# Optimization experiments

Hardware: AMD Instinct MI355X
Metric: run time of the kernel (lower is better)

## Reference

```python
import jax, jax.numpy as jnp
import numpy as np
from jax import lax

TAU = 1.0
GUMBEL_SCALE = 1e-4
SEARCH_SPACE = [1, 2, 4, 8, 16, 32, 64]


def synth_weight(weight, alphas_after):
    """Per-block circulant projection of weight for each block size, mixed by alphas.

    weight: [O, I, k, k]. For block size b: reshape to (q,b,p,b,k,k), rotate rows so
    each circulant diagonal aligns, mean over the block row axis, broadcast back with
    the reverse rotation, and accumulate alpha-weighted.
    """
    O, I, k, _ = weight.shape
    w = alphas_after[0] * weight  # block_size == 1 -> identity
    for idx, b in enumerate(SEARCH_SPACE[1:], start=1):
        q, p = O // b, I // b
        tmp = weight.reshape(q, b, p, b, k, k).transpose(0, 2, 1, 3, 4, 5)  # q,p,b,b,k,k
        ii = jnp.arange(b)[:, None]
        jj = jnp.arange(b)[None, :]
        rot = tmp[:, :, ii, (ii + jj) % b]          # q,p,b,b,k,k : rotate_mat gather
        cir = rot.mean(axis=2)                       # q,p,b,k,k   : circulant mean
        out = cir[:, :, (jj - ii) % b]               # q,p,b,b,k,k : rev_rotate_mat gather
        out = out.transpose(0, 2, 1, 3, 4, 5).reshape(O, I, k, k)
        w = w + alphas_after[idx] * out
    return w


def setup_inputs() -> dict:
    key = jax.random.key(0)
    k1, k2, k3 = jax.random.split(key, 3)
    B, C, H = 16, 256, 56
    O, I, K = 256, 256, 3
    x = jax.random.normal(k1, (B, C, H, H), dtype=jnp.float32)
    # kaiming-uniform-ish init: uniform in [-bound, bound], bound = sqrt(6/fan_in)
    fan_in = I * K * K
    bound = float(np.sqrt(6.0 / fan_in))
    weight = jax.random.uniform(k2, (O, I, K, K), dtype=jnp.float32, minval=-bound, maxval=bound)
    alphas = jnp.ones((len(SEARCH_SPACE),), dtype=jnp.float32)
    gumbels = jax.random.normal(k3, (len(SEARCH_SPACE),), dtype=jnp.float32)
    return {"x": x, "weight": weight, "alphas": alphas, "gumbels": gumbels}


def reference(x, weight, alphas, gumbels):
    # gumbel_softmax with tiny Gumbel(0, 1e-4) noise (noise passed in for determinism)
    alphas_after = jax.nn.softmax((alphas + GUMBEL_SCALE * gumbels) / TAU, axis=-1)
    w = synth_weight(weight, alphas_after)
    k = weight.shape[-1]
    pad = k // 2
    stride = 1
    out = lax.conv_general_dilated(
        x, w,
        window_strides=(stride, stride),
        padding=[(pad, pad), (pad, pad)],
        dimension_numbers=("NCHW", "OIHW", "NCHW"),
    )
    return out
```

## Files before the change

### kernel.cpp

```cpp
#include <hip/hip_runtime.h>
#include <hip/hip_bf16.h>

typedef __attribute__((ext_vector_type(8))) short bf16x8;
typedef __attribute__((ext_vector_type(4))) float f32x4;

#define WR_OFF   27557888

#define BAND     24576
#define WBUF_OFF 49152
#define WBUF_SZ  16384

__global__ void diagsum_kernel(const float* __restrict__ W, float* __restrict__ S) {
    int t = blockIdx.x * 256 + threadIdx.x;
    int idx, n, lvlOff;
    if (t < 32768)      { idx = 1; n = t;          lvlOff = 0; }
    else if (t < 49152) { idx = 2; n = t - 32768;  lvlOff = 294912; }
    else if (t < 57344) { idx = 3; n = t - 49152;  lvlOff = 442368; }
    else if (t < 61440) { idx = 4; n = t - 57344;  lvlOff = 516096; }
    else if (t < 63488) { idx = 5; n = t - 61440;  lvlOff = 552960; }
    else                { idx = 6; n = t - 63488;  lvlOff = 571392; }
    int b = 1 << idx;
    int d = n & (b - 1);
    int qp = n >> idx;
    int p = qp & ((256 >> idx) - 1);
    int q = qp >> (8 - idx);
    float s[9];
    #pragma unroll
    for (int tp = 0; tp < 9; ++tp) s[tp] = 0.f;
    for (int tt = 0; tt < b; ++tt) {
        const float* wp = W + ((size_t)((q * b + tt) * 256 + p * b + ((tt + d) & (b - 1)))) * 9;
        #pragma unroll
        for (int tp = 0; tp < 9; ++tp) s[tp] += wp[tp];
    }
    float* o = S + (size_t)lvlOff + (size_t)n * 9;
    #pragma unroll
    for (int tp = 0; tp < 9; ++tp) o[tp] = s[tp];
}

__global__ void wsynth_kernel(const float* __restrict__ W,
                              const float* __restrict__ alphas,
                              const float* __restrict__ gumbels,
                              const float* __restrict__ S,
                              __hip_bfloat16* __restrict__ Wr) {
    int tid = blockIdx.x * 256 + threadIdx.x;
    int o = tid >> 8, i = tid & 255;

    float a[7]; float mx = -1e30f;
    for (int j = 0; j < 7; ++j) { a[j] = alphas[j] + 1.0e-4f * gumbels[j]; mx = fmaxf(mx, a[j]); }
    float s = 0.f;
    for (int j = 0; j < 7; ++j) { a[j] = __expf(a[j] - mx); s += a[j]; }
    float invs = 1.0f / s;
    for (int j = 0; j < 7; ++j) a[j] *= invs;

    float acc[9];
    const float* w0 = W + ((size_t)(o * 256 + i)) * 9;
    #pragma unroll
    for (int t = 0; t < 9; ++t) acc[t] = a[0] * w0[t];

    const int lvlOff[7] = {0, 0, 294912, 442368, 516096, 552960, 571392};
    int dif = i - o;
    #pragma unroll
    for (int idx = 1; idx < 7; ++idx) {
        int b = 1 << idx;
        int q = o >> idx, p = i >> idx, d = dif & (b - 1);
        int n = ((q * (256 >> idx) + p) << idx) + d;
        const float* sp = S + lvlOff[idx] + (size_t)n * 9;
        float sc = a[idx] / (float)b;
        #pragma unroll
        for (int tp = 0; tp < 9; ++tp) acc[tp] += sc * sp[tp];
    }
    #pragma unroll
    for (int tp = 0; tp < 9; ++tp)
        Wr[((size_t)(tp * 256 + o)) * 256 + i] = __float2bfloat16(acc[tp]);
}

__global__ void zero_border_kernel(__hip_bfloat16* __restrict__ Xp) {
    int t = blockIdx.x * 256 + threadIdx.x;
    int c = t & 255;
    int pp = t >> 8;
    int b = pp / 228;
    int p = pp - b * 228;
    int y, x;
    if (p < 58)       { y = 0;            x = p; }
    else if (p < 116) { y = 57;           x = p - 58; }
    else if (p < 172) { y = 1 + (p - 116); x = 0; }
    else              { y = 1 + (p - 172); x = 57; }
    Xp[((size_t)(b * 58 + y) * 58 + x) * 256 + c] = __float2bfloat16(0.f);
}

__global__ void pad_nhwc_kernel(const float* __restrict__ x,
                                __hip_bfloat16* __restrict__ Xp) {
    __shared__ float t[64][65];
    int p0 = blockIdx.x * 64;
    int c0 = blockIdx.y * 64;
    int b  = blockIdx.z;
    int lane = threadIdx.x & 63;
    int grp  = threadIdx.x >> 6;

    const float* src = x + ((size_t)(b * 256 + c0)) * 3136 + p0;
    #pragma unroll
    for (int it = 0; it < 16; ++it) {
        int c = it * 4 + grp;
        t[c][lane] = src[(size_t)c * 3136 + lane];
    }
    __syncthreads();
    #pragma unroll
    for (int it = 0; it < 16; ++it) {
        int pl = it * 4 + grp;
        int P = p0 + pl;
        int y = P / 56, xx = P - y * 56;
        Xp[(((size_t)(b * 58 + y + 1)) * 58 + (xx + 1)) * 256 + c0 + lane] =
            __float2bfloat16(t[lane][pl]);
    }
}

__device__ __forceinline__ void gload16(const __hip_bfloat16* g, char* l) {
    __builtin_amdgcn_global_load_lds(
        (const __attribute__((address_space(1))) void*)g,
        (__attribute__((address_space(3))) void*)l, 16, 0, 0);
}

template<int N> __device__ __forceinline__ void gate() {
    if constexpr (N == 0)      asm volatile("s_waitcnt vmcnt(0)" ::: "memory");
    else if constexpr (N == 2) asm volatile("s_waitcnt vmcnt(2)" ::: "memory");
    else if constexpr (N == 4) asm volatile("s_waitcnt vmcnt(4)" ::: "memory");
    else if constexpr (N == 7) asm volatile("s_waitcnt vmcnt(7)" ::: "memory");
}

template<bool LAST>
__device__ __forceinline__ void chunk_body(
    int cc, char* smem,
    const int (&aOff)[4], const int (&bOff)[7],
    const __hip_bfloat16* wSrc0, const __hip_bfloat16* const (&xSrc)[3],
    int tid, f32x4 (&acc)[4][7])
{
    const char* xb = smem + (cc & 1) * BAND;
    #pragma unroll
    for (int r = 0; r < 9; ++r) {
        if (!LAST || r <= 5) {
            const int tap2 = (r < 6) ? r + 3 : r - 6;
            const int cc2  = (r < 6) ? cc : cc + 1;
            const __hip_bfloat16* s = wSrc0 + tap2 * 65536 + cc2 * 32;
            char* d = smem + WBUF_OFF + ((cc + r + 3) & 3) * WBUF_SZ + tid * 16;
            gload16(s, d);
            gload16(s + 16, d + 8192);
        }
        if (!LAST && r == 3) {
            char* d = smem + ((cc + 1) & 1) * BAND + tid * 16;
            #pragma unroll
            for (int it = 0; it < 3; ++it)
                gload16(xSrc[it] + (cc + 1) * 32, d + it * 8192);
        }
        const char* wb = smem + WBUF_OFF + ((cc + r) & 3) * WBUF_SZ;
        const int dy = r / 3 - 1, dx = r % 3 - 1;
        const int timm = (dy * 64 + dx) * 16;
        bf16x8 af[4], bfv[7];
        #pragma unroll
        for (int nf = 0; nf < 4; ++nf) af[nf] = *(const bf16x8*)(wb + aOff[nf]);
        #pragma unroll
        for (int mf = 0; mf < 7; ++mf) bfv[mf] = *(const bf16x8*)(xb + bOff[mf] + timm);
        __builtin_amdgcn_s_setprio(1);
        #pragma unroll
        for (int nf = 0; nf < 4; ++nf)
            #pragma unroll
            for (int mf = 0; mf < 7; ++mf)
                acc[nf][mf] = __builtin_amdgcn_mfma_f32_16x16x32_bf16(
                    af[nf], bfv[mf], acc[nf][mf], 0, 0, 0);
        __builtin_amdgcn_s_setprio(0);
        if constexpr (LAST) {
            if (r <= 5)      gate<4>();
            else if (r == 6) gate<2>();
            else if (r == 7) gate<0>();
        } else {
            if (r == 3 || r == 4 || r == 5) gate<7>();
            else                            gate<4>();
        }
        if (!(LAST && r == 8)) __builtin_amdgcn_s_barrier();
    }
}

__global__ __launch_bounds__(512, 2) void conv_kernel(
        const __hip_bfloat16* __restrict__ Xp,
        const __hip_bfloat16* __restrict__ Wr,
        float* __restrict__ out) {
    extern __shared__ char smem[];

    const int tid = threadIdx.x;
    const int w = tid >> 6, lane = tid & 63, l15 = lane & 15, q = lane >> 4;
    const int bid = blockIdx.x;
    const int bimg = bid / 14;
    const int y0 = (bid - bimg * 14) * 4;

    const int wn = (w & 3) << 6;
    const int wm = (w >> 2) * 112;

    const __hip_bfloat16* wSrc0 = Wr + (tid & 255) * 256 + (tid >> 8) * 8;

    const __hip_bfloat16* xSrc[3];
    #pragma unroll
    for (int it = 0; it < 3; ++it) {
        int chunk = tid + it * 512;
        int slot = chunk / 384;
        int rem  = chunk - slot * 384;
        int row = rem >> 6, xcol = rem & 63;
        xSrc[it] = Xp + (((size_t)(bimg * 58 + y0 + row)) * 58 + xcol) * 256 + slot * 8;
    }

    int aOff[4];
    #pragma unroll
    for (int nf = 0; nf < 4; ++nf) aOff[nf] = q * 4096 + (wn + nf * 16 + l15) * 16;
    int bOff[7];
    #pragma unroll
    for (int mf = 0; mf < 7; ++mf) {
        int p = wm + mf * 16 + l15;
        int y = p / 56, xx = p - y * 56;
        bOff[mf] = q * 6144 + ((y + 1) * 64 + (xx + 1)) * 16;
    }

    f32x4 acc[4][7];
    #pragma unroll
    for (int a1 = 0; a1 < 4; ++a1)
        #pragma unroll
        for (int a2 = 0; a2 < 7; ++a2)
            acc[a1][a2] = (f32x4){0.f, 0.f, 0.f, 0.f};

    {
        char* d = smem + tid * 16;
        #pragma unroll
        for (int it = 0; it < 3; ++it) gload16(xSrc[it], d + it * 8192);
        #pragma unroll
        for (int t = 0; t < 3; ++t) {
            const __hip_bfloat16* s = wSrc0 + t * 65536;
            char* dw = smem + WBUF_OFF + t * WBUF_SZ + tid * 16;
            gload16(s, dw);
            gload16(s + 16, dw + 8192);
        }
    }
    gate<4>();
    __builtin_amdgcn_s_barrier();

    for (int cc = 0; cc < 7; ++cc)
        chunk_body<false>(cc, smem, aOff, bOff, wSrc0, xSrc, tid, acc);
    chunk_body<true>(7, smem, aOff, bOff, wSrc0, xSrc, tid, acc);

    const int nb = wn + q * 4;
    const size_t obB = (size_t)bimg * 256 * 3136;
    #pragma unroll
    for (int mf = 0; mf < 7; ++mf) {
        int pm = y0 * 56 + wm + mf * 16 + l15;
        #pragma unroll
        for (int nf = 0; nf < 4; ++nf) {
            #pragma unroll
            for (int rr = 0; rr < 4; ++rr)
                out[obB + (size_t)(nb + nf * 16 + rr) * 3136 + pm] = acc[nf][mf][rr];
        }
    }
}

extern "C" void kernel_launch(void* const* d_in, const int* in_sizes, int n_in,
                              void* d_out, int out_size, void* d_ws, size_t ws_size,
                              hipStream_t stream) {
    const float* x       = (const float*)d_in[0];
    const float* weight  = (const float*)d_in[1];
    const float* alphas  = (const float*)d_in[2];
    const float* gumbels = (const float*)d_in[3];
    float* out = (float*)d_out;

    __hip_bfloat16* Xp = (__hip_bfloat16*)d_ws;
    float*          S  = (float*)d_ws;
    __hip_bfloat16* Wr = (__hip_bfloat16*)((char*)d_ws + WR_OFF);

    hipFuncSetAttribute(reinterpret_cast<const void*>(conv_kernel),
                        hipFuncAttributeMaxDynamicSharedMemorySize, 114688);

    hipLaunchKernelGGL(diagsum_kernel,     dim3(252),       dim3(256), 0, stream,
                       weight, S);
    hipLaunchKernelGGL(wsynth_kernel,      dim3(256),       dim3(256), 0, stream,
                       weight, alphas, gumbels, S, Wr);
    hipLaunchKernelGGL(zero_border_kernel, dim3(3648),      dim3(256), 0, stream, Xp);
    hipLaunchKernelGGL(pad_nhwc_kernel,    dim3(49, 4, 16), dim3(256), 0, stream, x, Xp);
    hipLaunchKernelGGL(conv_kernel,        dim3(224),       dim3(512), 114688, stream,
                       Xp, Wr, out);
}
```

Baseline: 111.0 us.

## Load conv weights directly into registers from fragment-ordered layout, drop LDS weight ring

The weight synthesis kernel now writes bf16 weights in an MFMA-fragment-friendly order, so the conv kernel reads A fragments straight from global memory into a double-buffered register set instead of staging them through a four-slot LDS ring. This removes most per-tap barriers and waitcnts and cuts LDS use to the two input bands, which may let more blocks fit per CU. The border-zeroing kernel is folded into the pad kernel to save a launch. The cost is that weight fetches now see global/L2 latency inside the MFMA loop, prefetched only one tap ahead.

```diff
diff --git a/kernel.cpp b/kernel.cpp
--- a/kernel.cpp
+++ b/kernel.cpp
@@ -6,9 +6,7 @@
 
 #define WR_OFF   27557888
 
-#define BAND     24576
-#define WBUF_OFF 49152
-#define WBUF_SZ  16384
+#define BAND 24576
 
 __global__ void diagsum_kernel(const float* __restrict__ W, float* __restrict__ S) {
     int t = blockIdx.x * 256 + threadIdx.x;
@@ -69,27 +67,30 @@
         #pragma unroll
         for (int tp = 0; tp < 9; ++tp) acc[tp] += sc * sp[tp];
     }
+    const size_t eb = (size_t)(i >> 5) * 8192 + ((i >> 3) & 3) * 2048 + o * 8 + (i & 7);
     #pragma unroll
     for (int tp = 0; tp < 9; ++tp)
-        Wr[((size_t)(tp * 256 + o)) * 256 + i] = __float2bfloat16(acc[tp]);
-}
-
-__global__ void zero_border_kernel(__hip_bfloat16* __restrict__ Xp) {
-    int t = blockIdx.x * 256 + threadIdx.x;
-    int c = t & 255;
-    int pp = t >> 8;
-    int b = pp / 228;
-    int p = pp - b * 228;
-    int y, x;
-    if (p < 58)       { y = 0;            x = p; }
-    else if (p < 116) { y = 57;           x = p - 58; }
-    else if (p < 172) { y = 1 + (p - 116); x = 0; }
-    else              { y = 1 + (p - 172); x = 57; }
-    Xp[((size_t)(b * 58 + y) * 58 + x) * 256 + c] = __float2bfloat16(0.f);
+        Wr[(size_t)tp * 65536 + eb] = __float2bfloat16(acc[tp]);
 }
 
 __global__ void pad_nhwc_kernel(const float* __restrict__ x,
                                 __hip_bfloat16* __restrict__ Xp) {
+    {
+        int bl = (blockIdx.z * 4 + blockIdx.y) * 49 + blockIdx.x;
+        int L = bl * 256 + threadIdx.x;
+        for (int e = L; e < 933888; e += 802816) {
+            int c = e & 255;
+            int pp = e >> 8;
+            int b = pp / 228;
+            int p = pp - b * 228;
+            int y, xx;
+            if (p < 58)       { y = 0;             xx = p; }
+            else if (p < 116) { y = 57;            xx = p - 58; }
+            else if (p < 172) { y = 1 + (p - 116); xx = 0; }
+            else              { y = 1 + (p - 172); xx = 57; }
+            Xp[((size_t)(b * 58 + y) * 58 + xx) * 256 + c] = __float2bfloat16(0.f);
+        }
+    }
     __shared__ float t[64][65];
     int p0 = blockIdx.x * 64;
     int c0 = blockIdx.y * 64;
@@ -122,60 +123,54 @@
 
 template<int N> __device__ __forceinline__ void gate() {
     if constexpr (N == 0)      asm volatile("s_waitcnt vmcnt(0)" ::: "memory");
-    else if constexpr (N == 2) asm volatile("s_waitcnt vmcnt(2)" ::: "memory");
     else if constexpr (N == 4) asm volatile("s_waitcnt vmcnt(4)" ::: "memory");
-    else if constexpr (N == 7) asm volatile("s_waitcnt vmcnt(7)" ::: "memory");
 }
 
 template<bool LAST>
-__device__ __forceinline__ void chunk_body(
-    int cc, char* smem,
-    const int (&aOff)[4], const int (&bOff)[7],
-    const __hip_bfloat16* wSrc0, const __hip_bfloat16* const (&xSrc)[3],
-    int tid, f32x4 (&acc)[4][7])
+__device__ __forceinline__ void chunk_pair(
+    int cp, char* smem, const char* aBase,
+    const int (&bOff)[7], const __hip_bfloat16* const (&xSrc)[3],
+    int tid, bf16x8 (&afr)[2][4], f32x4 (&acc)[4][7])
 {
-    const char* xb = smem + (cc & 1) * BAND;
-    #pragma unroll
-    for (int r = 0; r < 9; ++r) {
-        if (!LAST || r <= 5) {
-            const int tap2 = (r < 6) ? r + 3 : r - 6;
-            const int cc2  = (r < 6) ? cc : cc + 1;
-            const __hip_bfloat16* s = wSrc0 + tap2 * 65536 + cc2 * 32;
-            char* d = smem + WBUF_OFF + ((cc + r + 3) & 3) * WBUF_SZ + tid * 16;
-            gload16(s, d);
-            gload16(s + 16, d + 8192);
-        }
-        if (!LAST && r == 3) {
-            char* d = smem + ((cc + 1) & 1) * BAND + tid * 16;
-            #pragma unroll
-            for (int it = 0; it < 3; ++it)
-                gload16(xSrc[it] + (cc + 1) * 32, d + it * 8192);
-        }
-        const char* wb = smem + WBUF_OFF + ((cc + r) & 3) * WBUF_SZ;
-        const int dy = r / 3 - 1, dx = r % 3 - 1;
-        const int timm = (dy * 64 + dx) * 16;
-        bf16x8 af[4], bfv[7];
-        #pragma unroll
-        for (int nf = 0; nf < 4; ++nf) af[nf] = *(const bf16x8*)(wb + aOff[nf]);
-        #pragma unroll
-        for (int mf = 0; mf < 7; ++mf) bfv[mf] = *(const bf16x8*)(xb + bOff[mf] + timm);
-        __builtin_amdgcn_s_setprio(1);
-        #pragma unroll
-        for (int nf = 0; nf < 4; ++nf)
+    #pragma unroll
+    for (int u = 0; u < 2; ++u) {
+        const int cc = 2 * cp + u;
+        const char* xb = smem + u * BAND;
+        #pragma unroll
+        for (int r = 0; r < 9; ++r) {
+            const int cur = (u + r) & 1, nxt = cur ^ 1;
+            if (!(LAST && u == 1 && r == 8)) {
+                const int tapn = (r == 8) ? 0 : r + 1;
+                const int aoff = tapn * 131072 + (cc + (r == 8 ? 1 : 0)) * 16384;
+                #pragma unroll
+                for (int nf = 0; nf < 4; ++nf)
+                    afr[nxt][nf] = *(const bf16x8*)(aBase + aoff + nf * 256);
+            }
+            if (!(LAST && u == 1) && r == 3) {
+                char* d = smem + (u ^ 1) * BAND + tid * 16;
+                #pragma unroll
+                for (int it = 0; it < 3; ++it)
+                    gload16(xSrc[it] + (cc + 1) * 32, d + it * 8192);
+            }
+            const int dy = r / 3 - 1, dx = r % 3 - 1;
+            const int timm = (dy * 64 + dx) * 16;
+            bf16x8 bfv[7];
             #pragma unroll
             for (int mf = 0; mf < 7; ++mf)
-                acc[nf][mf] = __builtin_amdgcn_mfma_f32_16x16x32_bf16(
-                    af[nf], bfv[mf], acc[nf][mf], 0, 0, 0);
-        __builtin_amdgcn_s_setprio(0);
-        if constexpr (LAST) {
-            if (r <= 5)      gate<4>();
-            else if (r == 6) gate<2>();
-            else if (r == 7) gate<0>();
-        } else {
-            if (r == 3 || r == 4 || r == 5) gate<7>();
-            else                            gate<4>();
+                bfv[mf] = *(const bf16x8*)(xb + bOff[mf] + timm);
+            __builtin_amdgcn_s_setprio(1);
+            #pragma unroll
+            for (int nf = 0; nf < 4; ++nf)
+                #pragma unroll
+                for (int mf = 0; mf < 7; ++mf)
+                    acc[nf][mf] = __builtin_amdgcn_mfma_f32_16x16x32_bf16(
+                        afr[cur][nf], bfv[mf], acc[nf][mf], 0, 0, 0);
+            __builtin_amdgcn_s_setprio(0);
+            if (r == 8 && !(LAST && u == 1)) {
+                gate<4>();
+                __builtin_amdgcn_s_barrier();
+            }
         }
-        if (!(LAST && r == 8)) __builtin_amdgcn_s_barrier();
     }
 }
 
@@ -183,7 +178,7 @@
         const __hip_bfloat16* __restrict__ Xp,
         const __hip_bfloat16* __restrict__ Wr,
         float* __restrict__ out) {
-    extern __shared__ char smem[];
+    __shared__ char smem[2 * BAND];
 
     const int tid = threadIdx.x;
     const int w = tid >> 6, lane = tid & 63, l15 = lane & 15, q = lane >> 4;
@@ -194,7 +189,7 @@
     const int wn = (w & 3) << 6;
     const int wm = (w >> 2) * 112;
 
-    const __hip_bfloat16* wSrc0 = Wr + (tid & 255) * 256 + (tid >> 8) * 8;
+    const char* aBase = (const char*)Wr + q * 4096 + (wn + l15) * 16;
 
     const __hip_bfloat16* xSrc[3];
     #pragma unroll
@@ -206,9 +201,6 @@
         xSrc[it] = Xp + (((size_t)(bimg * 58 + y0 + row)) * 58 + xcol) * 256 + slot * 8;
     }
 
-    int aOff[4];
-    #pragma unroll
-    for (int nf = 0; nf < 4; ++nf) aOff[nf] = q * 4096 + (wn + nf * 16 + l15) * 16;
     int bOff[7];
     #pragma unroll
     for (int mf = 0; mf < 7; ++mf) {
@@ -224,24 +216,22 @@
         for (int a2 = 0; a2 < 7; ++a2)
             acc[a1][a2] = (f32x4){0.f, 0.f, 0.f, 0.f};
 
+    bf16x8 afr[2][4];
+
     {
         char* d = smem + tid * 16;
         #pragma unroll
         for (int it = 0; it < 3; ++it) gload16(xSrc[it], d + it * 8192);
-        #pragma unroll
-        for (int t = 0; t < 3; ++t) {
-            const __hip_bfloat16* s = wSrc0 + t * 65536;
-            char* dw = smem + WBUF_OFF + t * WBUF_SZ + tid * 16;
-            gload16(s, dw);
-            gload16(s + 16, dw + 8192);
-        }
-    }
-    gate<4>();
+    }
+    #pragma unroll
+    for (int nf = 0; nf < 4; ++nf)
+        afr[0][nf] = *(const bf16x8*)(aBase + nf * 256);
+    gate<0>();
     __builtin_amdgcn_s_barrier();
 
-    for (int cc = 0; cc < 7; ++cc)
-        chunk_body<false>(cc, smem, aOff, bOff, wSrc0, xSrc, tid, acc);
-    chunk_body<true>(7, smem, aOff, bOff, wSrc0, xSrc, tid, acc);
+    for (int cp = 0; cp < 3; ++cp)
+        chunk_pair<false>(cp, smem, aBase, bOff, xSrc, tid, afr, acc);
+    chunk_pair<true>(3, smem, aBase, bOff, xSrc, tid, afr, acc);
 
     const int nb = wn + q * 4;
     const size_t obB = (size_t)bimg * 256 * 3136;
@@ -270,15 +260,12 @@
     float*          S  = (float*)d_ws;
     __hip_bfloat16* Wr = (__hip_bfloat16*)((char*)d_ws + WR_OFF);
 
-    hipFuncSetAttribute(reinterpret_cast<const void*>(conv_kernel),
-                        hipFuncAttributeMaxDynamicSharedMemorySize, 114688);
-
-    hipLaunchKernelGGL(diagsum_kernel,     dim3(252),       dim3(256), 0, stream,
+    hipLaunchKernelGGL(diagsum_kernel,  dim3(252),       dim3(256), 0, stream,
                        weight, S);
-    hipLaunchKernelGGL(wsynth_kernel,      dim3(256),       dim3(256), 0, stream,
+    hipLaunchKernelGGL(wsynth_kernel,   dim3(256),       dim3(256), 0, stream,
                        weight, alphas, gumbels, S, Wr);
-    hipLaunchKernelGGL(zero_border_kernel, dim3(3648),      dim3(256), 0, stream, Xp);
-    hipLaunchKernelGGL(pad_nhwc_kernel,    dim3(49, 4, 16), dim3(256), 0, stream, x, Xp);
-    hipLaunchKernelGGL(conv_kernel,        dim3(224),       dim3(512), 114688, stream,
+    hipLaunchKernelGGL(pad_nhwc_kernel, dim3(49, 4, 16), dim3(256), 0, stream,
+                       x, Xp);
+    hipLaunchKernelGGL(conv_kernel,     dim3(224),       dim3(512), 0, stream,
                        Xp, Wr, out);
 }
```

Result: faster. 96.74 us (-12.9%).
